# Optimization experiments

Measured on AMD Instinct MI355X. Metric: run time of the kernel, lower is better.

Reference implementation:

```python
import jax, jax.numpy as jnp
import numpy as np

NEG = 16        # opt.negative_samples
K_PRED = 6      # opt.subcloud_cube_size - 2
B, C, D = 32, 256, 8
EPS = 1e-11


def _term(z, c, ignore, Wk, dim, k, skip, key):
    # one (dim, k) InfoNCE term
    ax = dim + 2                      # spatial axis in z/c
    s = k + skip
    L = z.shape[ax]
    z_sl = jax.lax.slice_in_dim(z, s, L, axis=ax)        # [B,C,d',h',w']
    c_sl = jax.lax.slice_in_dim(c, 0, L - s, axis=ax)    # [B,C,d',h',w']
    ig = (jax.lax.slice_in_dim(ignore, 0, L - s, axis=dim + 1)
          + jax.lax.slice_in_dim(ignore, s, L, axis=dim + 1))  # [B,d',h',w']

    # 1x1x1 Conv3d (no bias) == channel matmul
    ztwk = jnp.einsum('bcdhw,oc->dhwbo', z_sl, Wk)       # [d,h,w,B,O]
    d, h, w, b, o = ztwk.shape
    M = d * h * w * b
    flat = ztwk.reshape(M, o)
    # random negative sampling: same row index replicated across channels
    idx = jax.random.randint(key, (M * NEG,), 0, M)
    shuf = flat[idx].reshape(d, h, w, b, NEG, o)          # [d,h,w,B,N,O]

    ctx = jnp.transpose(c_sl, (2, 3, 4, 0, 1))            # [d,h,w,B,C]
    main = jnp.einsum('dhwbc,dhwbc->dhwb', ctx, ztwk)     # positive score
    negs = jnp.einsum('dhwbc,dhwbnc->dhwbn', ctx, shuf)   # negative scores
    scores = jnp.concatenate([main[..., None], negs], axis=-1)  # [d,h,w,B,1+N]

    probs = jax.nn.softmax(scores, axis=-1)
    logp0 = jnp.log(probs[..., 0] + EPS)                  # [d,h,w,B]
    nll = -jnp.transpose(logp0, (3, 0, 1, 2))             # [B,d,h,w]
    mask = (ig == 0)
    # NLL with target 0 everywhere, ignore_index on masked-out positions, mean reduction
    return (nll * mask).sum() / mask.sum()


def setup_inputs() -> dict:
    key = jax.random.key(0)
    kz, kc, kt, kw = jax.random.split(key, 4)
    z = jax.random.normal(kz, (B, C, D, D, D), dtype=jnp.float32)
    c = jax.random.normal(kc, (B, C, D, D, D), dtype=jnp.float32)
    targets_to_ignore = jax.random.randint(kt, (B, D, D, D), 0, 2, dtype=jnp.int32)
    Wk = jax.random.normal(kw, (K_PRED, C, C), dtype=jnp.float32) * 0.02  # [K,O,C]
    return {"z": z, "c": c, "targets_to_ignore": targets_to_ignore,
            "Wk": Wk, "skip_step": 1}


def reference(z, c, targets_to_ignore, Wk, skip_step):
    keys = jax.random.split(jax.random.key(42), 3 * K_PRED)
    total = jnp.float32(0.0)
    i = 0
    for dim in range(3):
        for k in range(1, K_PRED + 1):
            total = total + _term(z, c, targets_to_ignore, Wk[k - 1],
                                  dim, k, skip_step, keys[i])
            i += 1
    return total / (3 * K_PRED)
```

## Files before the change

kernel.cpp:

```cpp
#include <hip/hip_runtime.h>
#include <stdint.h>

#define EPSL 1e-11f

typedef _Float16 h2 __attribute__((ext_vector_type(2)));
typedef _Float16 h8 __attribute__((ext_vector_type(8)));
typedef __attribute__((ext_vector_type(4))) float f32x4;
typedef __attribute__((ext_vector_type(16))) float f32x16;

__device__ __forceinline__ uint32_t pk2h(float a, float b) {
    union { h2 h; uint32_t u; } t;
    t.h = (h2){ (_Float16)a, (_Float16)b };
    return t.u;
}
__device__ __forceinline__ uint16_t f2h(float a) {
    union { _Float16 h; uint16_t u; } t; t.h = (_Float16)a; return t.u;
}

__device__ __forceinline__ uint64_t sm64(uint64_t x) {
    x += 0x9E3779B97F4A7C15ULL;
    x = (x ^ (x >> 30)) * 0xBF58476D1CE4E5B9ULL;
    x = (x ^ (x >> 27)) * 0x94D049BB133111EBULL;
    return x ^ (x >> 31);
}

__device__ __forceinline__ uint32_t rowz_of(uint32_t f, int dim, int S, int s) {
    uint32_t b = f & 31u;
    uint32_t r = f >> 5;
    uint32_t d, h, w;
    if (dim == 0) {
        w = r & 7u; h = (r >> 3) & 7u; d = (r >> 6) + (uint32_t)s;
    } else if (dim == 1) {
        w = r & 7u; uint32_t q = r >> 3;
        h = q % (uint32_t)S + (uint32_t)s; d = q / (uint32_t)S;
    } else {
        w = r % (uint32_t)S + (uint32_t)s; uint32_t q = r / (uint32_t)S;
        h = q & 7u; d = q >> 3;
    }
    return b * 512u + d * 64u + h * 8u + w;
}

__global__ void k_init(float* sums_s, int* cnts_s) {
    int t = blockIdx.x * 256 + threadIdx.x;
    if (t < 1152) { sums_s[t] = 0.f; cnts_s[t] = 0; }
}

__global__ __launch_bounds__(256) void k_prep(const float* __restrict__ z,
                                              const float* __restrict__ c,
                                              uint16_t* __restrict__ zh,
                                              uint16_t* __restrict__ cTh) {
    __shared__ float tile[32][65];
    const int t = threadIdx.x;
    const int b = blockIdx.z & 31, isC = blockIdx.z >> 5;
    const float* src = (isC ? c : z) + (size_t)b * 131072;
    const int p0 = blockIdx.x * 64, ch0 = blockIdx.y * 32;
    const int pl = t & 63, cl0 = t >> 6;
    #pragma unroll
    for (int i = 0; i < 8; i++)
        tile[cl0 + i * 4][pl] = src[(ch0 + cl0 + i * 4) * 512 + p0 + pl];
    __syncthreads();
    const int ml = t >> 2, ck = (t & 3) * 8;
    uint4 o;
    o.x = pk2h(tile[ck + 0][ml], tile[ck + 1][ml]);
    o.y = pk2h(tile[ck + 2][ml], tile[ck + 3][ml]);
    o.z = pk2h(tile[ck + 4][ml], tile[ck + 5][ml]);
    o.w = pk2h(tile[ck + 6][ml], tile[ck + 7][ml]);
    uint16_t* dst = isC ? cTh : zh;
    *(uint4*)(dst + (size_t)(b * 512 + p0 + ml) * 256 + ch0 + ck) = o;
}

__global__ __launch_bounds__(256) void k_castw(const float* __restrict__ W,
                                               uint16_t* __restrict__ Whf) {
    const int gid = blockIdx.x * 4 + (threadIdx.x >> 6);
    const int lane = threadIdx.x & 63;
    const int kk = gid >> 7, rem = gid & 127;
    const int ks2 = rem >> 3, ot = rem & 7;
    const int o = ot * 32 + (lane & 31);
    const int cc = ks2 * 16 + (lane >> 5) * 8;
    const float* src = W + ((size_t)kk * 256 + o) * 256 + cc;
    float4 v0 = *(const float4*)src;
    float4 v1 = *(const float4*)(src + 4);
    uint4 out = make_uint4(pk2h(v0.x, v0.y), pk2h(v0.z, v0.w),
                           pk2h(v1.x, v1.y), pk2h(v1.z, v1.w));
    *(uint4*)(Whf + (size_t)gid * 512 + lane * 8) = out;
}

__global__ __launch_bounds__(256, 2) void k_gemm(const uint16_t* __restrict__ zh,
                                                 const uint16_t* __restrict__ Whf,
                                                 uint16_t* __restrict__ ZWh) {
    __shared__ uint16_t Bbuf[2][4096];
    __shared__ uint16_t Cbuf[4][4096];
    const int kk = blockIdx.y;
    const int t = threadIdx.x, lane = t & 63, wv = t >> 6;
    const int m0 = blockIdx.x * 128 + wv * 32;
    const int col = lane & 31, hl = lane >> 5;
    const uint16_t* W32 = Whf + (size_t)kk * 65536;
    const uint16_t* A0 = zh + (size_t)(m0 + col) * 256 + hl * 8;

    f32x16 acc[8];
    #pragma unroll
    for (int i = 0; i < 8; i++)
        #pragma unroll
        for (int jj = 0; jj < 16; jj++) acc[i][jj] = 0.f;

    {
        const uint16_t* src = W32 + t * 16;
        *(uint4*)(&Bbuf[0][t * 16]) = *(const uint4*)src;
        *(uint4*)(&Bbuf[0][t * 16 + 8]) = *(const uint4*)(src + 8);
    }
    __syncthreads();
    for (int ks2 = 0; ks2 < 16; ks2++) {
        if (ks2 < 15) {
            const uint16_t* src = W32 + (size_t)(ks2 + 1) * 4096 + t * 16;
            uint16_t* db = Bbuf[(ks2 + 1) & 1];
            *(uint4*)(&db[t * 16]) = *(const uint4*)src;
            *(uint4*)(&db[t * 16 + 8]) = *(const uint4*)(src + 8);
        }
        h8 a = *(const h8*)(A0 + ks2 * 16);
        const uint16_t* Bb = Bbuf[ks2 & 1];
        #pragma unroll
        for (int ot = 0; ot < 8; ot++) {
            h8 bv = *(const h8*)(&Bb[ot * 512 + lane * 8]);
            acc[ot] = __builtin_amdgcn_mfma_f32_32x32x16_f16(a, bv, acc[ot], 0, 0, 0);
        }
        __syncthreads();
    }

    uint16_t* Lb = Cbuf[wv];
    uint16_t* dstbase = ZWh + ((size_t)kk * 16384 + m0) * 256;
    #pragma unroll
    for (int hh = 0; hh < 2; hh++) {
        #pragma unroll
        for (int ot = 0; ot < 8; ot++)
            #pragma unroll
            for (int rg = 0; rg < 8; rg++) {
                int reg = hh * 8 + rg;
                int row = (reg & 3) + 8 * (reg >> 2) + 4 * hl;
                Lb[(row - hh * 16) * 256 + ot * 32 + col] = f2h(acc[ot][reg]);
            }
        const uint4* Lr = (const uint4*)Lb;
        uint4* dst = (uint4*)(dstbase + hh * 16 * 256);
        #pragma unroll
        for (int i = 0; i < 8; i++)
            dst[i * 64 + lane] = Lr[i * 64 + lane];
    }
}

__global__ __launch_bounds__(256, 4) void k_score(const uint16_t* __restrict__ ZWh,
                                                  const uint16_t* __restrict__ cTh,
                                                  const int* __restrict__ ign,
                                                  float* sums_s, int* cnts_s) {
    __shared__ float sbuf[4][288];
    __shared__ float wsum[4], wcnt[4];
    int bid = blockIdx.x;
    int kk = 0, cum = 0;
    for (;;) { int nb = 96 * (6 - kk); if (bid < cum + nb) break; cum += nb; kk++; }
    const int S = 6 - kk, T = S * 2048, s = kk + 2;
    const uint16_t* ZW = ZWh + (size_t)kk * 16384 * 256;

    const int local = bid - cum;
    const int dim = local / (32 * S);
    const int loc2 = local - dim * 32 * S;
    const int term = dim * 6 + kk;

    const int t = threadIdx.x, lane = t & 63, wv = t >> 6;
    const int lm = lane & 15, lq = lane >> 4;
    const uint32_t gidx = (uint32_t)(loc2 * 4 + wv);
    const uint32_t b = gidx & 31u;
    const uint32_t rb = gidx >> 5;
    const uint32_t r = rb * 16u + (uint32_t)lm;

    uint32_t d, h, w;
    if (dim == 0)      { w = r & 7u; h = (r >> 3) & 7u; d = r >> 6; }
    else if (dim == 1) { w = r & 7u; uint32_t qq = r >> 3; h = qq % (uint32_t)S; d = qq / (uint32_t)S; }
    else               { w = r % (uint32_t)S; uint32_t qq = r / (uint32_t)S; h = qq & 7u; d = qq >> 3; }
    uint32_t pc = d * 64u + h * 8u + w;
    uint32_t pz = pc + (dim == 0 ? (uint32_t)s * 64u : dim == 1 ? (uint32_t)s * 8u : (uint32_t)s);
    uint32_t rowc = b * 512u + pc;
    uint32_t rowz = b * 512u + pz;

    uint64_t x = sm64(((uint64_t)term << 40) +
                      (uint64_t)gidx * 128u + (uint64_t)lm);
    uint32_t nrow = rowz_of((uint32_t)(x >> 32) % (uint32_t)T, dim, S, s);

    int mok = (ign[rowc] + ign[rowz]) == 0;

    const uint16_t* cA = cTh + (size_t)rowc * 256 + lq * 8;
    const uint16_t* pB = ZW + (size_t)rowz * 256 + lq * 8;
    const uint16_t* nB = ZW + (size_t)nrow * 256 + lq * 8;

    h8 af[8], pf[8], nf[8];
    #pragma unroll
    for (int ks = 0; ks < 8; ks++) af[ks] = *(const h8*)(cA + ks * 32);
    #pragma unroll
    for (int ks = 0; ks < 8; ks++) pf[ks] = *(const h8*)(pB + ks * 32);
    #pragma unroll
    for (int ks = 0; ks < 8; ks++) nf[ks] = *(const h8*)(nB + ks * 32);

    f32x4 accp = (f32x4){0.f, 0.f, 0.f, 0.f};
    f32x4 accn = (f32x4){0.f, 0.f, 0.f, 0.f};
    #pragma unroll
    for (int ks = 0; ks < 8; ks++)
        accp = __builtin_amdgcn_mfma_f32_16x16x32_f16(af[ks], pf[ks], accp, 0, 0, 0);
    #pragma unroll
    for (int ks = 0; ks < 8; ks++)
        accn = __builtin_amdgcn_mfma_f32_16x16x32_f16(af[ks], nf[ks], accn, 0, 0, 0);

    float* Sb = sbuf[wv];
    #pragma unroll
    for (int rg = 0; rg < 4; rg++)
        Sb[(lq * 4 + rg) * 17 + lm] = accn[rg];
    if ((lm >> 2) == lq) Sb[272 + lm] = accp[lm & 3];

    float dpos = Sb[272 + lm];
    float mx = dpos;
    float scn[16];
    #pragma unroll
    for (int n = 0; n < 16; n++) { scn[n] = Sb[lm * 17 + n]; mx = fmaxf(mx, scn[n]); }
    float e0 = __expf(dpos - mx), sum = e0;
    #pragma unroll
    for (int n = 0; n < 16; n++) sum += __expf(scn[n] - mx);
    float nll = -__logf(e0 / sum + EPSL);

    float v = mok ? nll : 0.f;
    float cm = mok ? 1.f : 0.f;
    #pragma unroll
    for (int st = 1; st < 64; st <<= 1) {
        v  += __shfl_xor(v, st, 64);
        cm += __shfl_xor(cm, st, 64);
    }
    if (lane == 0) { wsum[wv] = v * 0.25f; wcnt[wv] = cm * 0.25f; }
    __syncthreads();
    if (t == 0) {
        float sv = wsum[0] + wsum[1] + wsum[2] + wsum[3];
        float cv = wcnt[0] + wcnt[1] + wcnt[2] + wcnt[3];
        int slot = blockIdx.x & 63;
        atomicAdd(&sums_s[term * 64 + slot], sv);
        atomicAdd(&cnts_s[term * 64 + slot], (int)(cv + 0.5f));
    }
}

__global__ void k_final(const float* __restrict__ sums_s, const int* __restrict__ cnts_s,
                        float* __restrict__ out) {
    __shared__ float ratio[18];
    int t = threadIdx.x;
    if (t < 18) {
        float sv = 0.f; int cv = 0;
        #pragma unroll 8
        for (int i = 0; i < 64; i++) { sv += sums_s[t * 64 + i]; cv += cnts_s[t * 64 + i]; }
        ratio[t] = sv / (float)cv;
    }
    __syncthreads();
    if (t == 0) {
        float tot = 0.f;
        #pragma unroll
        for (int i = 0; i < 18; i++) tot += ratio[i];
        out[0] = tot / 18.f;
    }
}

extern "C" void kernel_launch(void* const* d_in, const int* in_sizes, int n_in,
                              void* d_out, int out_size, void* d_ws, size_t ws_size,
                              hipStream_t stream) {
    const float* z   = (const float*)d_in[0];
    const float* c   = (const float*)d_in[1];
    const int*   ign = (const int*)d_in[2];
    const float* Wk  = (const float*)d_in[3];

    float* sums_s = (float*)d_ws;
    int*   cnts_s = (int*)((char*)d_ws + 4608);
    uint16_t* zh  = (uint16_t*)((char*)d_ws + 65536);
    uint16_t* cTh = zh  + (size_t)16384 * 256;
    uint16_t* Whf = cTh + (size_t)16384 * 256;
    uint16_t* ZWh = Whf + (size_t)6 * 65536;

    hipLaunchKernelGGL(k_init, dim3(5), dim3(256), 0, stream, sums_s, cnts_s);
    hipLaunchKernelGGL(k_prep, dim3(8, 8, 64), dim3(256), 0, stream, z, c, zh, cTh);
    hipLaunchKernelGGL(k_castw, dim3(192), dim3(256), 0, stream, Wk, Whf);
    hipLaunchKernelGGL(k_gemm, dim3(128, 6), dim3(256), 0, stream, zh, Whf, ZWh);
    hipLaunchKernelGGL(k_score, dim3(2016), dim3(256), 0, stream, ZWh, cTh, ign, sums_s, cnts_s);
    hipLaunchKernelGGL(k_final, dim3(1), dim3(64), 0, stream, sums_s, cnts_s, (float*)d_out);
}
```

Before: 142.3 us.

## Merge prep kernels into one launch and stage GEMM weights via direct-to-LDS loads

```diff
diff --git a/kernel.cpp b/kernel.cpp
--- a/kernel.cpp
+++ b/kernel.cpp
@@ -40,56 +40,58 @@
     return b * 512u + d * 64u + h * 8u + w;
 }
 
-__global__ void k_init(float* sums_s, int* cnts_s) {
-    int t = blockIdx.x * 256 + threadIdx.x;
-    if (t < 1152) { sums_s[t] = 0.f; cnts_s[t] = 0; }
-}
-
-__global__ __launch_bounds__(256) void k_prep(const float* __restrict__ z,
-                                              const float* __restrict__ c,
-                                              uint16_t* __restrict__ zh,
-                                              uint16_t* __restrict__ cTh) {
-    __shared__ float tile[32][65];
+
+__global__ __launch_bounds__(256) void k_prepall(const float* __restrict__ z,
+                                                 const float* __restrict__ c,
+                                                 const float* __restrict__ W,
+                                                 uint16_t* __restrict__ zh,
+                                                 uint16_t* __restrict__ cTh,
+                                                 uint16_t* __restrict__ Whf,
+                                                 float* sums_s, int* cnts_s) {
+    const int bid = blockIdx.x;
     const int t = threadIdx.x;
-    const int b = blockIdx.z & 31, isC = blockIdx.z >> 5;
-    const float* src = (isC ? c : z) + (size_t)b * 131072;
-    const int p0 = blockIdx.x * 64, ch0 = blockIdx.y * 32;
-    const int pl = t & 63, cl0 = t >> 6;
-    #pragma unroll
-    for (int i = 0; i < 8; i++)
-        tile[cl0 + i * 4][pl] = src[(ch0 + cl0 + i * 4) * 512 + p0 + pl];
-    __syncthreads();
-    const int ml = t >> 2, ck = (t & 3) * 8;
-    uint4 o;
-    o.x = pk2h(tile[ck + 0][ml], tile[ck + 1][ml]);
-    o.y = pk2h(tile[ck + 2][ml], tile[ck + 3][ml]);
-    o.z = pk2h(tile[ck + 4][ml], tile[ck + 5][ml]);
-    o.w = pk2h(tile[ck + 6][ml], tile[ck + 7][ml]);
-    uint16_t* dst = isC ? cTh : zh;
-    *(uint4*)(dst + (size_t)(b * 512 + p0 + ml) * 256 + ch0 + ck) = o;
-}
-
-__global__ __launch_bounds__(256) void k_castw(const float* __restrict__ W,
-                                               uint16_t* __restrict__ Whf) {
-    const int gid = blockIdx.x * 4 + (threadIdx.x >> 6);
-    const int lane = threadIdx.x & 63;
-    const int kk = gid >> 7, rem = gid & 127;
-    const int ks2 = rem >> 3, ot = rem & 7;
-    const int o = ot * 32 + (lane & 31);
-    const int cc = ks2 * 16 + (lane >> 5) * 8;
-    const float* src = W + ((size_t)kk * 256 + o) * 256 + cc;
-    float4 v0 = *(const float4*)src;
-    float4 v1 = *(const float4*)(src + 4);
-    uint4 out = make_uint4(pk2h(v0.x, v0.y), pk2h(v0.z, v0.w),
-                           pk2h(v1.x, v1.y), pk2h(v1.z, v1.w));
-    *(uint4*)(Whf + (size_t)gid * 512 + lane * 8) = out;
+    if (bid < 4096) {
+        __shared__ float tile[32][65];
+        const int zz = bid >> 6;
+        const int b = zz & 31, isC = zz >> 5;
+        const float* src = (isC ? c : z) + (size_t)b * 131072;
+        const int p0 = (bid & 7) * 64, ch0 = ((bid >> 3) & 7) * 32;
+        const int pl = t & 63, cl0 = t >> 6;
+        #pragma unroll
+        for (int i = 0; i < 8; i++)
+            tile[cl0 + i * 4][pl] = src[(ch0 + cl0 + i * 4) * 512 + p0 + pl];
+        __syncthreads();
+        const int ml = t >> 2, ck = (t & 3) * 8;
+        uint4 o;
+        o.x = pk2h(tile[ck + 0][ml], tile[ck + 1][ml]);
+        o.y = pk2h(tile[ck + 2][ml], tile[ck + 3][ml]);
+        o.z = pk2h(tile[ck + 4][ml], tile[ck + 5][ml]);
+        o.w = pk2h(tile[ck + 6][ml], tile[ck + 7][ml]);
+        uint16_t* dst = isC ? cTh : zh;
+        *(uint4*)(dst + (size_t)(b * 512 + p0 + ml) * 256 + ch0 + ck) = o;
+    } else if (bid < 4288) {
+        const int gid = (bid - 4096) * 4 + (t >> 6);
+        const int lane = t & 63;
+        const int kk = gid >> 7, rem = gid & 127;
+        const int ks2 = rem >> 3, ot = rem & 7;
+        const int o = ot * 32 + (lane & 31);
+        const int cc = ks2 * 16 + (lane >> 5) * 8;
+        const float* src = W + ((size_t)kk * 256 + o) * 256 + cc;
+        float4 v0 = *(const float4*)src;
+        float4 v1 = *(const float4*)(src + 4);
+        uint4 out = make_uint4(pk2h(v0.x, v0.y), pk2h(v0.z, v0.w),
+                               pk2h(v1.x, v1.y), pk2h(v1.z, v1.w));
+        *(uint4*)(Whf + (size_t)gid * 512 + lane * 8) = out;
+    } else {
+        int t2 = (bid - 4288) * 256 + t;
+        if (t2 < 1152) { sums_s[t2] = 0.f; cnts_s[t2] = 0; }
+    }
 }
 
 __global__ __launch_bounds__(256, 2) void k_gemm(const uint16_t* __restrict__ zh,
                                                  const uint16_t* __restrict__ Whf,
                                                  uint16_t* __restrict__ ZWh) {
-    __shared__ uint16_t Bbuf[2][4096];
-    __shared__ uint16_t Cbuf[4][4096];
+    __shared__ __align__(16) uint16_t smem[16384];
     const int kk = blockIdx.y;
     const int t = threadIdx.x, lane = t & 63, wv = t >> 6;
     const int m0 = blockIdx.x * 128 + wv * 32;
@@ -103,30 +105,38 @@
         #pragma unroll
         for (int jj = 0; jj < 16; jj++) acc[i][jj] = 0.f;
 
-    {
-        const uint16_t* src = W32 + t * 16;
-        *(uint4*)(&Bbuf[0][t * 16]) = *(const uint4*)src;
-        *(uint4*)(&Bbuf[0][t * 16 + 8]) = *(const uint4*)(src + 8);
-    }
+    #define BSTAGE(sk_, buf_) { \
+        const char* gb_ = (const char*)W32 + (size_t)(sk_) * 16384 + wv * 4096 + lane * 16; \
+        char* lb_ = (char*)smem + (buf_) * 16384 + wv * 4096; \
+        _Pragma("unroll") \
+        for (int i_ = 0; i_ < 4; i_++) \
+            __builtin_amdgcn_global_load_lds( \
+                (const __attribute__((address_space(1))) void*)(gb_ + i_ * 1024), \
+                (__attribute__((address_space(3))) void*)(lb_ + i_ * 1024), 16, 0, 0); \
+    }
+
+    BSTAGE(0, 0);
+    asm volatile("s_waitcnt vmcnt(0)" ::: "memory");
     __syncthreads();
-    for (int ks2 = 0; ks2 < 16; ks2++) {
-        if (ks2 < 15) {
-            const uint16_t* src = W32 + (size_t)(ks2 + 1) * 4096 + t * 16;
-            uint16_t* db = Bbuf[(ks2 + 1) & 1];
-            *(uint4*)(&db[t * 16]) = *(const uint4*)src;
-            *(uint4*)(&db[t * 16 + 8]) = *(const uint4*)(src + 8);
+    for (int sk = 0; sk < 8; sk++) {
+        if (sk < 7) BSTAGE(sk + 1, (sk + 1) & 1);
+        const uint16_t* Bb = smem + (sk & 1) * 8192;
+        #pragma unroll
+        for (int half = 0; half < 2; half++) {
+            h8 a = *(const h8*)(A0 + (sk * 2 + half) * 16);
+            const uint16_t* Bh = Bb + half * 4096;
+            #pragma unroll
+            for (int ot = 0; ot < 8; ot++) {
+                h8 bv = *(const h8*)(&Bh[ot * 512 + lane * 8]);
+                acc[ot] = __builtin_amdgcn_mfma_f32_32x32x16_f16(a, bv, acc[ot], 0, 0, 0);
+            }
         }
-        h8 a = *(const h8*)(A0 + ks2 * 16);
-        const uint16_t* Bb = Bbuf[ks2 & 1];
-        #pragma unroll
-        for (int ot = 0; ot < 8; ot++) {
-            h8 bv = *(const h8*)(&Bb[ot * 512 + lane * 8]);
-            acc[ot] = __builtin_amdgcn_mfma_f32_32x32x16_f16(a, bv, acc[ot], 0, 0, 0);
-        }
+        asm volatile("s_waitcnt vmcnt(0)" ::: "memory");
         __syncthreads();
     }
-
-    uint16_t* Lb = Cbuf[wv];
+    #undef BSTAGE
+
+    uint16_t* Lb = smem + wv * 4096;
     uint16_t* dstbase = ZWh + ((size_t)kk * 16384 + m0) * 256;
     #pragma unroll
     for (int hh = 0; hh < 2; hh++) {
@@ -274,9 +284,8 @@
     uint16_t* Whf = cTh + (size_t)16384 * 256;
     uint16_t* ZWh = Whf + (size_t)6 * 65536;
 
-    hipLaunchKernelGGL(k_init, dim3(5), dim3(256), 0, stream, sums_s, cnts_s);
-    hipLaunchKernelGGL(k_prep, dim3(8, 8, 64), dim3(256), 0, stream, z, c, zh, cTh);
-    hipLaunchKernelGGL(k_castw, dim3(192), dim3(256), 0, stream, Wk, Whf);
+    hipLaunchKernelGGL(k_prepall, dim3(4293), dim3(256), 0, stream,
+                       z, c, Wk, zh, cTh, Whf, sums_s, cnts_s);
     hipLaunchKernelGGL(k_gemm, dim3(128, 6), dim3(256), 0, stream, zh, Whf, ZWh);
     hipLaunchKernelGGL(k_score, dim3(2016), dim3(256), 0, stream, ZWh, cTh, ign, sums_s, cnts_s);
     hipLaunchKernelGGL(k_final, dim3(1), dim3(64), 0, stream, sums_s, cnts_s, (float*)d_out);
```

Measured after the change: 129.0 us. -9.4%, faster.
